# Optimization experiments

Hardware: AMD Instinct MI355X
Metric: run time of the kernel (lower is better)

## Reference

```python
import jax, jax.numpy as jnp
import numpy as np

A_BITS = 16
W_BITS = 8
KH = KW = 3
STRIDE = 1
PADDING = 1


def fake_quant(x, bits, axes=None):
    """Asymmetric min/max fake quantization with straight-through estimator."""
    if axes is None:
        mn = x.min()
        mx = x.max()
    else:
        mn = x.min(axis=axes, keepdims=True)
        mx = x.max(axis=axes, keepdims=True)
    qmax = float(2 ** bits - 1)
    scale = jnp.maximum((mx - mn) / qmax, 1e-12)
    zp = jnp.round(-mn / scale)
    q = jnp.clip(jnp.round(x / scale) + zp, 0.0, qmax)
    deq = (q - zp) * scale
    # STE: identity gradient through the quantizer
    return x + jax.lax.stop_gradient(deq - x)


def unfold(x, kh, kw, stride, padding):
    """torch.nn.functional.unfold equivalent -> (N, C*kh*kw, Hout*Wout)."""
    N, C, H, W = x.shape
    xp = jnp.pad(x, ((0, 0), (0, 0), (padding, padding), (padding, padding)))
    Ho = (H - kh + 2 * padding) // stride + 1
    Wo = (W - kw + 2 * padding) // stride + 1
    cols = []
    for i in range(kh):          # small fixed 3x3 loop
        for j in range(kw):
            cols.append(xp[:, :, i:i + Ho * stride:stride, j:j + Wo * stride:stride])
    xcol = jnp.stack(cols, axis=2)              # (N, C, kh*kw, Ho, Wo)
    return xcol.reshape(N, C * kh * kw, Ho * Wo), Ho, Wo


def adder_op(W_col, X_col):
    # W_col: (F, K), X_col: (K, L) -> out: (F, L); L1-distance "conv"
    return -jnp.abs(W_col[:, :, None] - X_col[None, :, :]).sum(axis=1)


def setup_inputs() -> dict:
    key = jax.random.key(0)
    kx, kw = jax.random.split(key)
    x = jax.random.normal(kx, (4, 64, 28, 28), dtype=jnp.float32)
    W = jax.random.normal(kw, (64, 64, 3, 3), dtype=jnp.float32)
    return {"x": x, "W": W}


def reference(x, W):
    # first_layer == 0 -> activation fake-quant; per-channel weight fake-quant
    qx = fake_quant(x, A_BITS)
    qw = fake_quant(W, W_BITS, axes=(1, 2, 3))
    N = x.shape[0]
    F = W.shape[0]
    xcol, Ho, Wo = unfold(qx, KH, KW, STRIDE, PADDING)   # (N, K, L0)
    K = xcol.shape[1]
    # torch: permute(1,2,0).view(K, L0*N) -> batch fastest within a row
    X_col = jnp.transpose(xcol, (1, 2, 0)).reshape(K, -1)  # (K, L0*N)
    W_col = qw.reshape(F, K)
    out = adder_op(W_col, X_col)                            # (F, L0*N)
    out = out.reshape(F, Ho, Wo, N).transpose(3, 0, 1, 2)   # (N, F, Ho, Wo)
    return out
```

## Files before the change

kernel.cpp:

```cpp
#include <hip/hip_runtime.h>
#include <math.h>

#define N_  4
#define C_  64
#define H_  28
#define W_  28
#define F_  64
#define KK  576
#define NX  (N_*C_*H_*W_)
#define NX4 (NX/4)

#define CH_STRIDE 100


__global__ __launch_bounds__(256) void k_prep(const float* __restrict__ x,
                                              const float* __restrict__ Wg,
                                              float* __restrict__ ws) {
  __shared__ float sm[4], sM[4];
  int tid = threadIdx.x, lane = tid & 63, wv = tid >> 6;

  const float4* x4 = (const float4*)x;
  float m = 3.4e38f, M = -3.4e38f;
  for (int i = blockIdx.x * 256 + tid; i < NX4; i += 64 * 256) {
    float4 v = x4[i];
    m = fminf(m, fminf(fminf(v.x, v.y), fminf(v.z, v.w)));
    M = fmaxf(M, fmaxf(fmaxf(v.x, v.y), fmaxf(v.z, v.w)));
  }
  #pragma unroll
  for (int o = 32; o; o >>= 1) {
    m = fminf(m, __shfl_xor(m, o));
    M = fmaxf(M, __shfl_xor(M, o));
  }
  if (lane == 0) { sm[wv] = m; sM[wv] = M; }
  __syncthreads();
  if (tid == 0) {
    m = fminf(fminf(sm[0], sm[1]), fminf(sm[2], sm[3]));
    M = fmaxf(fmaxf(sM[0], sM[1]), fmaxf(sM[2], sM[3]));
    ws[blockIdx.x] = m;
    ws[64 + blockIdx.x] = M;
  }

  if (blockIdx.x < 16) {
    int f = blockIdx.x * 4 + wv;
    const float* wp = Wg + f * KK;
    float v[9];
    float wm = 3.4e38f, wM = -3.4e38f;
    #pragma unroll
    for (int u = 0; u < 9; ++u) {
      v[u] = wp[lane + 64 * u];
      wm = fminf(wm, v[u]);
      wM = fmaxf(wM, v[u]);
    }
    #pragma unroll
    for (int o = 32; o; o >>= 1) {
      wm = fminf(wm, __shfl_xor(wm, o));
      wM = fmaxf(wM, __shfl_xor(wM, o));
    }
    float s = fmaxf((wM - wm) / 255.0f, 1e-12f);
    float z = rintf(-wm / s);
    float rs = 1.0f / s;
    float* Wt = ws + 256;
    #pragma unroll
    for (int u = 0; u < 9; ++u) {
      float q = fminf(fmaxf(rintf(v[u] * rs) + z, 0.0f), 255.0f);
      Wt[(lane + 64 * u) * 64 + f] = (q - z) * s;
    }
  }
}

__global__ __launch_bounds__(256, 1) void k_main(const float* __restrict__ x,
                                                 const float* __restrict__ ws,
                                                 float* __restrict__ out) {
  __shared__ __align__(16) float Xs[64 * CH_STRIDE];
  __shared__ float Rbuf[16 * 32 * 29];
  int tid = threadIdx.x;
  int lane = tid & 63;
  int fl = tid & 15, cq = tid >> 4;
  int y = blockIdx.x, n = blockIdx.y, fh = blockIdx.z;

  float m = ws[lane], M = ws[64 + lane];
  #pragma unroll
  for (int o = 32; o; o >>= 1) {
    m = fminf(m, __shfl_xor(m, o));
    M = fmaxf(M, __shfl_xor(M, o));
  }
  float sx = fmaxf((M - m) / 65535.0f, 1e-12f);
  float zx = rintf(-m / sx);
  float rx = 1.0f / sx;

  for (int idx = tid; idx < 64 * 3 * 30; idx += 256) {
    int c = idx / 90, rem = idx - c * 90;
    int r = rem / 30, p = rem - r * 30;
    int row = y + r - 1, col = p - 1;
    float v = 0.0f;
    if ((unsigned)row < 28u && (unsigned)col < 28u) {
      float raw = x[((n * 64 + c) * 28 + row) * 28 + col];
      float q = fminf(fmaxf(rintf(raw * rx) + zx, 0.0f), 65535.0f);
      v = (q - zx) * sx;
    }
    Xs[c * CH_STRIDE + r * 32 + p] = v;
  }
  __syncthreads();

  const float* Wt = ws + 256;
  int f0 = fh * 32 + fl;
  float acc0[28], acc1[28];
  #pragma unroll
  for (int i = 0; i < 28; ++i) { acc0[i] = 0.0f; acc1[i] = 0.0f; }

  float wc[18], wn[18];
  {
    const float* wp = Wt + (cq * 9) * 64 + f0;
    #pragma unroll
    for (int k = 0; k < 9; ++k) { wn[k] = wp[k * 64]; wn[9 + k] = wp[k * 64 + 16]; }
  }

  for (int ci = 0; ci < 4; ++ci) {
    #pragma unroll
    for (int k = 0; k < 18; ++k) wc[k] = wn[k];
    if (ci < 3) {
      int cn = cq + 16 * (ci + 1);
      const float* wp = Wt + (cn * 9) * 64 + f0;
      #pragma unroll
      for (int k = 0; k < 9; ++k) { wn[k] = wp[k * 64]; wn[9 + k] = wp[k * 64 + 16]; }
    }
    int c = cq + 16 * ci;
    #pragma unroll
    for (int r = 0; r < 3; ++r) {
      const float4* xr4 = (const float4*)&Xs[c * CH_STRIDE + r * 32];
      float xv[32];
      #pragma unroll
      for (int i = 0; i < 8; ++i) ((float4*)xv)[i] = xr4[i];
      float wa0 = wc[3 * r], wa1 = wc[3 * r + 1], wa2 = wc[3 * r + 2];
      float wb0 = wc[9 + 3 * r], wb1 = wc[9 + 3 * r + 1], wb2 = wc[9 + 3 * r + 2];
      #pragma unroll
      for (int p = 0; p < 28; ++p) {
        acc0[p] += fabsf(wa0 - xv[p]) + fabsf(wa1 - xv[p + 1]) + fabsf(wa2 - xv[p + 2]);
        acc1[p] += fabsf(wb0 - xv[p]) + fabsf(wb1 - xv[p + 1]) + fabsf(wb2 - xv[p + 2]);
      }
    }
  }

  #pragma unroll
  for (int p = 0; p < 28; ++p) {
    Rbuf[(cq * 32 + fl) * 29 + p] = acc0[p];
    Rbuf[(cq * 32 + fl + 16) * 29 + p] = acc1[p];
  }
  __syncthreads();

  #pragma unroll
  for (int i = 0; i < 4; ++i) {
    int idx = tid + 256 * i;
    if (idx < 896) {
      int ff = idx / 28, col = idx - ff * 28;
      float s = 0.0f;
      #pragma unroll
      for (int q = 0; q < 16; ++q) s += Rbuf[(q * 32 + ff) * 29 + col];
      out[((n * 64 + fh * 32 + ff) * 28 + y) * 28 + col] = -s;
    }
  }
}

extern "C" void kernel_launch(void* const* d_in, const int* in_sizes, int n_in,
                              void* d_out, int out_size, void* d_ws, size_t ws_size,
                              hipStream_t stream) {
  const float* x  = (const float*)d_in[0];
  const float* Wg = (const float*)d_in[1];
  float* out = (float*)d_out;
  float* ws  = (float*)d_ws;

  hipLaunchKernelGGL(k_prep, dim3(64), dim3(256), 0, stream, x, Wg, ws);
  hipLaunchKernelGGL(k_main, dim3(28, 4, 2), dim3(256), 0, stream, x, ws, out);
}
```

Measured before the change: 80.58 us.

## Split output row into column halves to double grid and raise occupancy

Each block now computes 14 output columns instead of 28, with the grid z dimension doubled to cover both column halves. Shared buffers and per-thread accumulators shrink, and launch bounds allow two blocks per CU. The intent is to fill more compute units and improve latency hiding. The cost is duplicated weight loads and halo reloads of the input per block.

```diff
diff --git a/kernel.cpp b/kernel.cpp
--- a/kernel.cpp
+++ b/kernel.cpp
@@ -10,7 +10,7 @@
 #define NX  (N_*C_*H_*W_)
 #define NX4 (NX/4)
 
-#define CH_STRIDE 100
+#define XCH 52
 
 
 __global__ __launch_bounds__(256) void k_prep(const float* __restrict__ x,
@@ -68,15 +68,17 @@
   }
 }
 
-__global__ __launch_bounds__(256, 1) void k_main(const float* __restrict__ x,
+__global__ __launch_bounds__(256, 2) void k_main(const float* __restrict__ x,
                                                  const float* __restrict__ ws,
                                                  float* __restrict__ out) {
-  __shared__ __align__(16) float Xs[64 * CH_STRIDE];
-  __shared__ float Rbuf[16 * 32 * 29];
+  __shared__ __align__(16) float Xs[64 * XCH];
+  __shared__ float Rbuf[16 * 32 * 15];
   int tid = threadIdx.x;
   int lane = tid & 63;
   int fl = tid & 15, cq = tid >> 4;
-  int y = blockIdx.x, n = blockIdx.y, fh = blockIdx.z;
+  int y = blockIdx.x, n = blockIdx.y;
+  int fh = blockIdx.z >> 1, colh = blockIdx.z & 1;
+  int bc = colh * 14;
 
   float m = ws[lane], M = ws[64 + lane];
   #pragma unroll
@@ -88,25 +90,29 @@
   float zx = rintf(-m / sx);
   float rx = 1.0f / sx;
 
-  for (int idx = tid; idx < 64 * 3 * 30; idx += 256) {
-    int c = idx / 90, rem = idx - c * 90;
-    int r = rem / 30, p = rem - r * 30;
-    int row = y + r - 1, col = p - 1;
-    float v = 0.0f;
-    if ((unsigned)row < 28u && (unsigned)col < 28u) {
-      float raw = x[((n * 64 + c) * 28 + row) * 28 + col];
-      float q = fminf(fmaxf(rintf(raw * rx) + zx, 0.0f), 65535.0f);
-      v = (q - zx) * sx;
+  {
+    int j = tid & 15, sub = tid >> 4;
+    #pragma unroll
+    for (int it = 0; it < 12; ++it) {
+      int cr = sub + 16 * it;
+      int c = cr / 3, r = cr - c * 3;
+      int row = y + r - 1, col = bc - 1 + j;
+      float v = 0.0f;
+      if ((unsigned)row < 28u && (unsigned)col < 28u) {
+        float raw = x[((n * 64 + c) * 28 + row) * 28 + col];
+        float q = fminf(fmaxf(rintf(raw * rx) + zx, 0.0f), 65535.0f);
+        v = (q - zx) * sx;
+      }
+      Xs[c * XCH + r * 16 + j] = v;
     }
-    Xs[c * CH_STRIDE + r * 32 + p] = v;
   }
   __syncthreads();
 
   const float* Wt = ws + 256;
   int f0 = fh * 32 + fl;
-  float acc0[28], acc1[28];
+  float acc0[14], acc1[14];
   #pragma unroll
-  for (int i = 0; i < 28; ++i) { acc0[i] = 0.0f; acc1[i] = 0.0f; }
+  for (int i = 0; i < 14; ++i) { acc0[i] = 0.0f; acc1[i] = 0.0f; }
 
   float wc[18], wn[18];
   {
@@ -119,22 +125,21 @@
     #pragma unroll
     for (int k = 0; k < 18; ++k) wc[k] = wn[k];
     if (ci < 3) {
-      int cn = cq + 16 * (ci + 1);
-      const float* wp = Wt + (cn * 9) * 64 + f0;
+      const float* wp = Wt + ((cq + 16 * (ci + 1)) * 9) * 64 + f0;
       #pragma unroll
       for (int k = 0; k < 9; ++k) { wn[k] = wp[k * 64]; wn[9 + k] = wp[k * 64 + 16]; }
     }
     int c = cq + 16 * ci;
     #pragma unroll
     for (int r = 0; r < 3; ++r) {
-      const float4* xr4 = (const float4*)&Xs[c * CH_STRIDE + r * 32];
-      float xv[32];
+      const float4* xr4 = (const float4*)&Xs[c * XCH + r * 16];
+      float xv[16];
       #pragma unroll
-      for (int i = 0; i < 8; ++i) ((float4*)xv)[i] = xr4[i];
+      for (int i = 0; i < 4; ++i) ((float4*)xv)[i] = xr4[i];
       float wa0 = wc[3 * r], wa1 = wc[3 * r + 1], wa2 = wc[3 * r + 2];
       float wb0 = wc[9 + 3 * r], wb1 = wc[9 + 3 * r + 1], wb2 = wc[9 + 3 * r + 2];
       #pragma unroll
-      for (int p = 0; p < 28; ++p) {
+      for (int p = 0; p < 14; ++p) {
         acc0[p] += fabsf(wa0 - xv[p]) + fabsf(wa1 - xv[p + 1]) + fabsf(wa2 - xv[p + 2]);
         acc1[p] += fabsf(wb0 - xv[p]) + fabsf(wb1 - xv[p + 1]) + fabsf(wb2 - xv[p + 2]);
       }
@@ -142,21 +147,21 @@
   }
 
   #pragma unroll
-  for (int p = 0; p < 28; ++p) {
-    Rbuf[(cq * 32 + fl) * 29 + p] = acc0[p];
-    Rbuf[(cq * 32 + fl + 16) * 29 + p] = acc1[p];
+  for (int p = 0; p < 14; ++p) {
+    Rbuf[(cq * 32 + fl) * 15 + p]      = acc0[p];
+    Rbuf[(cq * 32 + 16 + fl) * 15 + p] = acc1[p];
   }
   __syncthreads();
 
   #pragma unroll
-  for (int i = 0; i < 4; ++i) {
+  for (int i = 0; i < 2; ++i) {
     int idx = tid + 256 * i;
-    if (idx < 896) {
-      int ff = idx / 28, col = idx - ff * 28;
+    if (idx < 448) {
+      int ff = idx / 14, col = idx - ff * 14;
       float s = 0.0f;
       #pragma unroll
-      for (int q = 0; q < 16; ++q) s += Rbuf[(q * 32 + ff) * 29 + col];
-      out[((n * 64 + fh * 32 + ff) * 28 + y) * 28 + col] = -s;
+      for (int q = 0; q < 16; ++q) s += Rbuf[(q * 32 + ff) * 15 + col];
+      out[((n * 64 + fh * 32 + ff) * 28 + y) * 28 + bc + col] = -s;
     }
   }
 }
@@ -170,5 +175,5 @@
   float* ws  = (float*)d_ws;
 
   hipLaunchKernelGGL(k_prep, dim3(64), dim3(256), 0, stream, x, Wg, ws);
-  hipLaunchKernelGGL(k_main, dim3(28, 4, 2), dim3(256), 0, stream, x, ws, out);
+  hipLaunchKernelGGL(k_main, dim3(28, 4, 4), dim3(256), 0, stream, x, ws, out);
 }
```

Result: faster. 73.69 us (-8.6%).
